# Optimization experiments

Hardware: AMD Instinct MI355X
Metric: run time of the kernel (lower is better)

## Reference

```python
import jax, jax.numpy as jnp
import numpy as np

T, TOPK = 512, 2
E, H, D = 8, 2816, 1024


def setup_inputs() -> dict:
    key = jax.random.key(0)
    k1, k2, k3, k4, k5 = jax.random.split(key, 5)
    x = jax.random.normal(k1, (T, D), dtype=jnp.float32)
    expert_indices = jax.random.randint(k2, (T, TOPK), 0, E, dtype=jnp.int64)
    w1 = jax.random.normal(k3, (E, H, D), dtype=jnp.float32)
    w2 = jax.random.normal(k4, (E, H, D), dtype=jnp.float32)
    w3 = jax.random.normal(k5, (E, H, D), dtype=jnp.float32)
    return {"x": x, "expert_indices": expert_indices, "w1": w1, "w2": w2, "w3": w3}


def reference(x, expert_indices, w1, w2, w3):
    # Math identical to: silu(x @ w1[e].T) * (x @ w3[e].T) @ w2[e] for e = expert_indices[t, a].
    # Computed densely over all experts (GEMM-friendly), then gathered per token,
    # which avoids materializing [T, a, H, D] gathered weight tensors.
    h1 = jax.nn.silu(jnp.einsum('ti,ehi->teh', x, w1))   # [T, E, H]
    h3 = jnp.einsum('ti,ehi->teh', x, w3)                # [T, E, H]
    out_all = jnp.einsum('teh,ehi->tei', h1 * h3, w2)    # [T, E, D]
    # gather the top_k selected experts per token -> [T, TOPK, D]
    idx = expert_indices[:, :, None]                     # [T, a, 1]
    expert_outs = jnp.take_along_axis(out_all, idx, axis=1)
    return expert_outs
```

## Files before the change

kernel.cpp:

```cpp
#include <hip/hip_runtime.h>


#define NEXP 8
#define HDIM 2816
#define DDIM 1024
#define NPAIR 1024

typedef unsigned int uint;
typedef unsigned short ushort;
typedef __attribute__((ext_vector_type(8))) short bf16x8;
typedef __attribute__((ext_vector_type(4))) float fvec4;
typedef __attribute__((ext_vector_type(4))) uint uvec4;

__device__ __forceinline__ ushort f2bf(float f) {
    uint u = __builtin_bit_cast(uint, f);
    u += 0x7fff + ((u >> 16) & 1);
    return (ushort)(u >> 16);
}
__device__ __forceinline__ uint pack2(float lo, float hi) {
    return (uint)f2bf(lo) | ((uint)f2bf(hi) << 16);
}
__device__ __forceinline__ uvec4 pack8(fvec4 a, fvec4 b) {
    uvec4 v;
    v.x = pack2(a.x, a.y); v.y = pack2(a.z, a.w);
    v.z = pack2(b.x, b.y); v.w = pack2(b.z, b.w);
    return v;
}

__device__ __forceinline__ void wg_sync_lds() {
    __builtin_amdgcn_sched_barrier(0);
    asm volatile("s_waitcnt lgkmcnt(0)" ::: "memory");
    __builtin_amdgcn_s_barrier();
    __builtin_amdgcn_sched_barrier(0);
}

__global__ __launch_bounds__(1024) void route_kernel(const int* __restrict__ idx,
                                                     int* __restrict__ counts,
                                                     int* __restrict__ lists) {
    int p = threadIdx.x;
    if (p < NEXP) counts[p] = 0;
    __syncthreads();
    int e = idx[p];
    int pos = atomicAdd(&counts[e], 1);
    lists[e * NPAIR + pos] = p;
}

#define LDB 68
#define NCH1 (DDIM / 64)

__global__ __launch_bounds__(512, 3) void h_mfma(const float* __restrict__ x,
                       const float* __restrict__ w1,
                       const float* __restrict__ w3,
                       const int* __restrict__ counts,
                       const int* __restrict__ lists,
                       ushort* __restrict__ hb) {
    const int e = blockIdx.x;
    const int cnt = counts[e];
    const int m0 = blockIdx.z * 128;
    if (m0 >= cnt) return;
    const int h0 = blockIdx.y * 64;

    __shared__ ushort sB1[2][64 * LDB];
    __shared__ ushort sB3[2][64 * LDB];
    __shared__ int sTok[128];
    __shared__ int sPairS[128];

    const int tid = threadIdx.x;
    if (tid < 128) {
        int m = m0 + tid;
        int mc = (m < cnt) ? m : (cnt - 1);
        int p = lists[e * NPAIR + mc];
        sTok[tid] = p >> 1;
        sPairS[tid] = (m < cnt) ? p : -1;
    }

    const int w = tid >> 6;
    const int lane = tid & 63;
    const int l16 = lane & 15;
    const int quad = lane >> 4;

    const int brow = tid >> 3;
    const int bc = (tid & 7) * 8;
    const float* pB1 = w1 + (size_t)e * HDIM * DDIM + (size_t)(h0 + brow) * DDIM + bc;
    const float* pB3 = w3 + (size_t)e * HDIM * DDIM + (size_t)(h0 + brow) * DDIM + bc;

    fvec4 pf[2][4];

#define P1_ISSUE(S, KC) do { \
    const float* q1 = pB1 + (KC) * 64; \
    const float* q3 = pB3 + (KC) * 64; \
    pf[S][0] = *(const fvec4*)q1;  pf[S][1] = *(const fvec4*)(q1 + 4); \
    pf[S][2] = *(const fvec4*)q3;  pf[S][3] = *(const fvec4*)(q3 + 4); \
} while (0)

#define P1_STAGE(S, B) do { \
    *(uvec4*)&sB1[B][brow * LDB + bc] = pack8(pf[S][0], pf[S][1]); \
    *(uvec4*)&sB3[B][brow * LDB + bc] = pack8(pf[S][2], pf[S][3]); \
} while (0)

    P1_ISSUE(0, 0);
    P1_ISSUE(1, 1);
    wg_sync_lds();
    const float* xA = x + (size_t)sTok[w * 16 + l16] * DDIM + quad * 8;

    fvec4 acc1[4], acc3[4];
    #pragma unroll
    for (int i = 0; i < 4; ++i) { acc1[i] = (fvec4)0.f; acc3[i] = (fvec4)0.f; }

    P1_STAGE(0, 0);
    wg_sync_lds();

#define P1_BODY(T, CUR) do { \
    const int kA = (T) * 64; \
    fvec4 a0 = *(const fvec4*)(xA + kA); \
    fvec4 a1 = *(const fvec4*)(xA + kA + 4); \
    fvec4 a2 = *(const fvec4*)(xA + kA + 32); \
    fvec4 a3 = *(const fvec4*)(xA + kA + 36); \
    if ((T) + 2 < NCH1) P1_ISSUE(CUR, (T) + 2); \
    bf16x8 af0 = __builtin_bit_cast(bf16x8, pack8(a0, a1)); \
    bf16x8 af1 = __builtin_bit_cast(bf16x8, pack8(a2, a3)); \
    _Pragma("unroll") \
    for (int ni = 0; ni < 4; ++ni) { \
        const int ro = (ni * 16 + l16) * LDB + quad * 8; \
        bf16x8 b10 = *(const bf16x8*)&sB1[CUR][ro]; \
        bf16x8 b30 = *(const bf16x8*)&sB3[CUR][ro]; \
        bf16x8 b11 = *(const bf16x8*)&sB1[CUR][ro + 32]; \
        bf16x8 b31 = *(const bf16x8*)&sB3[CUR][ro + 32]; \
        acc1[ni] = __builtin_amdgcn_mfma_f32_16x16x32_bf16(af0, b10, acc1[ni], 0, 0, 0); \
        acc3[ni] = __builtin_amdgcn_mfma_f32_16x16x32_bf16(af0, b30, acc3[ni], 0, 0, 0); \
        acc1[ni] = __builtin_amdgcn_mfma_f32_16x16x32_bf16(af1, b11, acc1[ni], 0, 0, 0); \
        acc3[ni] = __builtin_amdgcn_mfma_f32_16x16x32_bf16(af1, b31, acc3[ni], 0, 0, 0); \
    } \
    if ((T) + 1 < NCH1) { \
        P1_STAGE(CUR ^ 1, CUR ^ 1); \
        wg_sync_lds(); \
    } \
} while (0)

    for (int t = 0; t < NCH1; t += 2) {
        P1_BODY(t, 0);
        P1_BODY(t + 1, 1);
    }

    #pragma unroll
    for (int r = 0; r < 4; ++r) {
        int m = w * 16 + quad * 4 + r;
        int p = sPairS[m];
        if (p >= 0) {
            size_t base = (size_t)p * HDIM + h0;
            #pragma unroll
            for (int ni = 0; ni < 4; ++ni) {
                float a = acc1[ni][r];
                float g = acc3[ni][r];
                float s = a / (1.f + __expf(-a)) * g;
                hb[base + ni * 16 + l16] = f2bf(s);
            }
        }
    }
}

#define LDB2 68
#define NCH2 ((HDIM / 4) / 64)

__global__ __launch_bounds__(512, 3) void out_mfma(const float* __restrict__ w2,
                         const int* __restrict__ counts,
                         const int* __restrict__ lists,
                         const ushort* __restrict__ hb,
                         float* __restrict__ out) {
    const int e = blockIdx.x;
    const int cnt = counts[e];
    const int mb = blockIdx.z >> 2;
    const int sk = blockIdx.z & 3;
    const int m0 = mb * 128;
    if (m0 >= cnt) return;
    const int n0 = blockIdx.y * 64;
    const int kbase = sk * (HDIM / 4);

    __shared__ ushort sB[2][64 * LDB2];
    __shared__ int sPairC[128];
    __shared__ int sPairS[128];

    const int tid = threadIdx.x;
    if (tid < 128) {
        int m = m0 + tid;
        int mc = (m < cnt) ? m : (cnt - 1);
        int p = lists[e * NPAIR + mc];
        sPairC[tid] = p;
        sPairS[tid] = (m < cnt) ? p : -1;
    }

    const int w = tid >> 6;
    const int lane = tid & 63;
    const int l16 = lane & 15;
    const int quad = lane >> 4;
    const int kp = tid >> 4;
    const int n4 = tid & 15;

    const float* pW = w2 + (size_t)e * HDIM * DDIM
                         + (size_t)(kbase + 2 * kp) * DDIM + n0 + n4 * 4;

    fvec4 pw[2][2];

#define P2_ISSUE(S, KC) do { \
    const float* q = pW + (size_t)(KC) * 64 * DDIM; \
    pw[S][0] = *(const fvec4*)q; \
    pw[S][1] = *(const fvec4*)(q + DDIM); \
} while (0)

#define P2_STAGE(S, B) do { \
    _Pragma("unroll") \
    for (int j = 0; j < 4; ++j) \
        *(uint*)&sB[B][(n4 * 4 + j) * LDB2 + kp * 2] = pack2(pw[S][0][j], pw[S][1][j]); \
} while (0)

    P2_ISSUE(0, 0);
    P2_ISSUE(1, 1);
    wg_sync_lds();
    const ushort* pA = hb + (size_t)sPairC[w * 16 + l16] * HDIM + kbase + quad * 8;

    fvec4 acc[4];
    #pragma unroll
    for (int i = 0; i < 4; ++i) acc[i] = (fvec4)0.f;

    P2_STAGE(0, 0);
    wg_sync_lds();

#define P2_BODY(T, CUR) do { \
    const int kA = (T) * 64; \
    bf16x8 af0 = *(const bf16x8*)(pA + kA); \
    bf16x8 af1 = *(const bf16x8*)(pA + kA + 32); \
    if ((T) + 2 < NCH2) P2_ISSUE(CUR, (T) + 2); \
    _Pragma("unroll") \
    for (int ni = 0; ni < 4; ++ni) { \
        const int ro = (ni * 16 + l16) * LDB2 + quad * 8; \
        bf16x8 b0 = *(const bf16x8*)&sB[CUR][ro]; \
        bf16x8 b1 = *(const bf16x8*)&sB[CUR][ro + 32]; \
        acc[ni] = __builtin_amdgcn_mfma_f32_16x16x32_bf16(af0, b0, acc[ni], 0, 0, 0); \
        acc[ni] = __builtin_amdgcn_mfma_f32_16x16x32_bf16(af1, b1, acc[ni], 0, 0, 0); \
    } \
    if ((T) + 1 < NCH2) { \
        P2_STAGE(CUR ^ 1, CUR ^ 1); \
        wg_sync_lds(); \
    } \
} while (0)

    for (int t = 0; t < NCH2; t += 2) {
        P2_BODY(t, 0);
        if (t + 1 < NCH2) P2_BODY(t + 1, 1);
    }

    #pragma unroll
    for (int r = 0; r < 4; ++r) {
        int m = w * 16 + quad * 4 + r;
        int p = sPairS[m];
        if (p >= 0) {
            #pragma unroll
            for (int ni = 0; ni < 4; ++ni)
                atomicAdd(&out[(size_t)p * DDIM + n0 + ni * 16 + l16], acc[ni][r]);
        }
    }
}

extern "C" void kernel_launch(void* const* d_in, const int* in_sizes, int n_in,
                              void* d_out, int out_size, void* d_ws, size_t ws_size,
                              hipStream_t stream) {
    const float* x   = (const float*)d_in[0];
    const int*   idx = (const int*)d_in[1];
    const float* w1  = (const float*)d_in[2];
    const float* w2  = (const float*)d_in[3];
    const float* w3  = (const float*)d_in[4];
    float* out = (float*)d_out;

    char* ws = (char*)d_ws;
    int*    counts = (int*)ws;
    int*    lists  = (int*)(ws + 1024);
    ushort* hbuf   = (ushort*)(ws + 65536);

    hipMemsetAsync(out, 0, (size_t)out_size * sizeof(float), stream);
    route_kernel<<<1, NPAIR, 0, stream>>>(idx, counts, lists);
    h_mfma<<<dim3(NEXP, HDIM / 64, NPAIR / 128), 512, 0, stream>>>(
        x, w1, w3, counts, lists, hbuf);
    out_mfma<<<dim3(NEXP, DDIM / 64, (NPAIR / 128) * 4), 512, 0, stream>>>(
        w2, counts, lists, hbuf, out);
}
```

Before: 330.1 us.

## Stage A tiles through LDS and shrink N tiles to 32 in both MoE GEMMs

Both expert GEMM kernels now load the activation rows (x or the bf16 hidden buffer) cooperatively into a double-buffered LDS tile. Before, each wave read its A fragments straight from global memory. The output-column tile is halved from 64 to 32, which doubles the grid, and waves are rearranged as a 4x2 grid over M and N, each computing 32x16 per matrix. Launch bounds now ask for 4 blocks per CU instead of 3. The aim is more parallelism and coalesced A loads. The cost is that x/hb rows are reloaded twice as many times across blocks, and fewer MFMAs run per LDS read.

Result: slower. 345.2 us (+4.6%).

```diff
diff --git a/kernel.cpp b/kernel.cpp
--- a/kernel.cpp
+++ b/kernel.cpp
@@ -45,10 +45,11 @@
     lists[e * NPAIR + pos] = p;
 }
 
-#define LDB 68
+#define LDK 68
+
 #define NCH1 (DDIM / 64)
 
-__global__ __launch_bounds__(512, 3) void h_mfma(const float* __restrict__ x,
+__global__ __launch_bounds__(512, 4) void h_mfma(const float* __restrict__ x,
                        const float* __restrict__ w1,
                        const float* __restrict__ w3,
                        const int* __restrict__ counts,
@@ -58,10 +59,10 @@
     const int cnt = counts[e];
     const int m0 = blockIdx.z * 128;
     if (m0 >= cnt) return;
-    const int h0 = blockIdx.y * 64;
-
-    __shared__ ushort sB1[2][64 * LDB];
-    __shared__ ushort sB3[2][64 * LDB];
+    const int h0 = blockIdx.y * 32;
+
+    __shared__ ushort sA[2][128 * LDK];
+    __shared__ ushort sB[2][2][32 * LDK];
     __shared__ int sTok[128];
     __shared__ int sPairS[128];
 
@@ -73,64 +74,75 @@
         sTok[tid] = p >> 1;
         sPairS[tid] = (m < cnt) ? p : -1;
     }
+    wg_sync_lds();
+
+    const int arow = tid >> 2;
+    const int akg  = (tid & 3) * 16;
+    const float* aSrc = x + (size_t)sTok[arow] * DDIM + akg;
+
+    const int bmat = tid >> 8;
+    const int brow = (tid >> 3) & 31;
+    const int bkg  = (tid & 7) * 8;
+    const float* bSrc = (bmat ? w3 : w1) + (size_t)e * HDIM * DDIM
+                        + (size_t)(h0 + brow) * DDIM + bkg;
+
+    fvec4 pfA[2][4];
+    fvec4 pfB[2][2];
+
+#define P1_ISSUE(S, KC) do { \
+    const float* qa = aSrc + (KC) * 64; \
+    pfA[S][0] = *(const fvec4*)qa; \
+    pfA[S][1] = *(const fvec4*)(qa + 4); \
+    pfA[S][2] = *(const fvec4*)(qa + 8); \
+    pfA[S][3] = *(const fvec4*)(qa + 12); \
+    const float* qb = bSrc + (KC) * 64; \
+    pfB[S][0] = *(const fvec4*)qb; \
+    pfB[S][1] = *(const fvec4*)(qb + 4); \
+} while (0)
+
+#define P1_STAGE(S, B) do { \
+    *(uvec4*)&sA[B][arow * LDK + akg] = pack8(pfA[S][0], pfA[S][1]); \
+    *(uvec4*)&sA[B][arow * LDK + akg + 8] = pack8(pfA[S][2], pfA[S][3]); \
+    *(uvec4*)&sB[B][bmat][brow * LDK + bkg] = pack8(pfB[S][0], pfB[S][1]); \
+} while (0)
 
     const int w = tid >> 6;
+    const int wm = w & 3;
+    const int wh = w >> 2;
     const int lane = tid & 63;
     const int l16 = lane & 15;
     const int quad = lane >> 4;
 
-    const int brow = tid >> 3;
-    const int bc = (tid & 7) * 8;
-    const float* pB1 = w1 + (size_t)e * HDIM * DDIM + (size_t)(h0 + brow) * DDIM + bc;
-    const float* pB3 = w3 + (size_t)e * HDIM * DDIM + (size_t)(h0 + brow) * DDIM + bc;
-
-    fvec4 pf[2][4];
-
-#define P1_ISSUE(S, KC) do { \
-    const float* q1 = pB1 + (KC) * 64; \
-    const float* q3 = pB3 + (KC) * 64; \
-    pf[S][0] = *(const fvec4*)q1;  pf[S][1] = *(const fvec4*)(q1 + 4); \
-    pf[S][2] = *(const fvec4*)q3;  pf[S][3] = *(const fvec4*)(q3 + 4); \
-} while (0)
-
-#define P1_STAGE(S, B) do { \
-    *(uvec4*)&sB1[B][brow * LDB + bc] = pack8(pf[S][0], pf[S][1]); \
-    *(uvec4*)&sB3[B][brow * LDB + bc] = pack8(pf[S][2], pf[S][3]); \
-} while (0)
+    const int ar0 = (wm * 32 + l16) * LDK + quad * 8;
+    const int br0 = (wh * 16 + l16) * LDK + quad * 8;
+
+    fvec4 acc[2][2];
+    #pragma unroll
+    for (int i = 0; i < 2; ++i) { acc[i][0] = (fvec4)0.f; acc[i][1] = (fvec4)0.f; }
 
     P1_ISSUE(0, 0);
     P1_ISSUE(1, 1);
-    wg_sync_lds();
-    const float* xA = x + (size_t)sTok[w * 16 + l16] * DDIM + quad * 8;
-
-    fvec4 acc1[4], acc3[4];
-    #pragma unroll
-    for (int i = 0; i < 4; ++i) { acc1[i] = (fvec4)0.f; acc3[i] = (fvec4)0.f; }
-
     P1_STAGE(0, 0);
     wg_sync_lds();
 
 #define P1_BODY(T, CUR) do { \
-    const int kA = (T) * 64; \
-    fvec4 a0 = *(const fvec4*)(xA + kA); \
-    fvec4 a1 = *(const fvec4*)(xA + kA + 4); \
-    fvec4 a2 = *(const fvec4*)(xA + kA + 32); \
-    fvec4 a3 = *(const fvec4*)(xA + kA + 36); \
+    bf16x8 a00 = *(const bf16x8*)&sA[CUR][ar0]; \
+    bf16x8 a01 = *(const bf16x8*)&sA[CUR][ar0 + 32]; \
+    bf16x8 a10 = *(const bf16x8*)&sA[CUR][ar0 + 16 * LDK]; \
+    bf16x8 a11 = *(const bf16x8*)&sA[CUR][ar0 + 16 * LDK + 32]; \
+    bf16x8 b00 = *(const bf16x8*)&sB[CUR][0][br0]; \
+    bf16x8 b01 = *(const bf16x8*)&sB[CUR][0][br0 + 32]; \
+    bf16x8 b10 = *(const bf16x8*)&sB[CUR][1][br0]; \
+    bf16x8 b11 = *(const bf16x8*)&sB[CUR][1][br0 + 32]; \
     if ((T) + 2 < NCH1) P1_ISSUE(CUR, (T) + 2); \
-    bf16x8 af0 = __builtin_bit_cast(bf16x8, pack8(a0, a1)); \
-    bf16x8 af1 = __builtin_bit_cast(bf16x8, pack8(a2, a3)); \
-    _Pragma("unroll") \
-    for (int ni = 0; ni < 4; ++ni) { \
-        const int ro = (ni * 16 + l16) * LDB + quad * 8; \
-        bf16x8 b10 = *(const bf16x8*)&sB1[CUR][ro]; \
-        bf16x8 b30 = *(const bf16x8*)&sB3[CUR][ro]; \
-        bf16x8 b11 = *(const bf16x8*)&sB1[CUR][ro + 32]; \
-        bf16x8 b31 = *(const bf16x8*)&sB3[CUR][ro + 32]; \
-        acc1[ni] = __builtin_amdgcn_mfma_f32_16x16x32_bf16(af0, b10, acc1[ni], 0, 0, 0); \
-        acc3[ni] = __builtin_amdgcn_mfma_f32_16x16x32_bf16(af0, b30, acc3[ni], 0, 0, 0); \
-        acc1[ni] = __builtin_amdgcn_mfma_f32_16x16x32_bf16(af1, b11, acc1[ni], 0, 0, 0); \
-        acc3[ni] = __builtin_amdgcn_mfma_f32_16x16x32_bf16(af1, b31, acc3[ni], 0, 0, 0); \
-    } \
+    acc[0][0] = __builtin_amdgcn_mfma_f32_16x16x32_bf16(a00, b00, acc[0][0], 0, 0, 0); \
+    acc[0][1] = __builtin_amdgcn_mfma_f32_16x16x32_bf16(a00, b10, acc[0][1], 0, 0, 0); \
+    acc[1][0] = __builtin_amdgcn_mfma_f32_16x16x32_bf16(a10, b00, acc[1][0], 0, 0, 0); \
+    acc[1][1] = __builtin_amdgcn_mfma_f32_16x16x32_bf16(a10, b10, acc[1][1], 0, 0, 0); \
+    acc[0][0] = __builtin_amdgcn_mfma_f32_16x16x32_bf16(a01, b01, acc[0][0], 0, 0, 0); \
+    acc[0][1] = __builtin_amdgcn_mfma_f32_16x16x32_bf16(a01, b11, acc[0][1], 0, 0, 0); \
+    acc[1][0] = __builtin_amdgcn_mfma_f32_16x16x32_bf16(a11, b01, acc[1][0], 0, 0, 0); \
+    acc[1][1] = __builtin_amdgcn_mfma_f32_16x16x32_bf16(a11, b11, acc[1][1], 0, 0, 0); \
     if ((T) + 1 < NCH1) { \
         P1_STAGE(CUR ^ 1, CUR ^ 1); \
         wg_sync_lds(); \
@@ -143,26 +155,24 @@
     }
 
     #pragma unroll
-    for (int r = 0; r < 4; ++r) {
-        int m = w * 16 + quad * 4 + r;
-        int p = sPairS[m];
-        if (p >= 0) {
-            size_t base = (size_t)p * HDIM + h0;
-            #pragma unroll
-            for (int ni = 0; ni < 4; ++ni) {
-                float a = acc1[ni][r];
-                float g = acc3[ni][r];
+    for (int mi = 0; mi < 2; ++mi) {
+        #pragma unroll
+        for (int r = 0; r < 4; ++r) {
+            int mrow = wm * 32 + mi * 16 + quad * 4 + r;
+            int p = sPairS[mrow];
+            if (p >= 0) {
+                float a = acc[mi][0][r];
+                float g = acc[mi][1][r];
                 float s = a / (1.f + __expf(-a)) * g;
-                hb[base + ni * 16 + l16] = f2bf(s);
+                hb[(size_t)p * HDIM + h0 + wh * 16 + l16] = f2bf(s);
             }
         }
     }
 }
 
-#define LDB2 68
 #define NCH2 ((HDIM / 4) / 64)
 
-__global__ __launch_bounds__(512, 3) void out_mfma(const float* __restrict__ w2,
+__global__ __launch_bounds__(512, 4) void out_mfma(const float* __restrict__ w2,
                          const int* __restrict__ counts,
                          const int* __restrict__ lists,
                          const ushort* __restrict__ hb,
@@ -173,10 +183,11 @@
     const int sk = blockIdx.z & 3;
     const int m0 = mb * 128;
     if (m0 >= cnt) return;
-    const int n0 = blockIdx.y * 64;
+    const int n0 = blockIdx.y * 32;
     const int kbase = sk * (HDIM / 4);
 
-    __shared__ ushort sB[2][64 * LDB2];
+    __shared__ ushort sA[2][128 * LDK];
+    __shared__ ushort sB[2][32 * LDK];
     __shared__ int sPairC[128];
     __shared__ int sPairS[128];
 
@@ -188,56 +199,71 @@
         sPairC[tid] = p;
         sPairS[tid] = (m < cnt) ? p : -1;
     }
+    wg_sync_lds();
+
+    const int arow = tid >> 2;
+    const int akg  = (tid & 3) * 16;
+    const ushort* aSrc = hb + (size_t)sPairC[arow] * HDIM + kbase + akg;
+
+    const int bkp = (tid >> 3) & 31;
+    const int bdg = tid & 7;
+    const float* bSrc = w2 + (size_t)e * HDIM * DDIM
+                        + (size_t)(kbase + 2 * bkp) * DDIM + n0 + bdg * 4;
+
+    uvec4 pfA[2][2];
+    fvec4 pfB[2][2];
+
+#define P2_ISSUE(S, KC) do { \
+    const ushort* qa = aSrc + (KC) * 64; \
+    pfA[S][0] = *(const uvec4*)qa; \
+    pfA[S][1] = *(const uvec4*)(qa + 8); \
+    if (tid < 256) { \
+        const float* qb = bSrc + (size_t)(KC) * 64 * DDIM; \
+        pfB[S][0] = *(const fvec4*)qb; \
+        pfB[S][1] = *(const fvec4*)(qb + DDIM); \
+    } \
+} while (0)
+
+#define P2_STAGE(S, B) do { \
+    *(uvec4*)&sA[B][arow * LDK + akg] = pfA[S][0]; \
+    *(uvec4*)&sA[B][arow * LDK + akg + 8] = pfA[S][1]; \
+    if (tid < 256) { \
+        _Pragma("unroll") \
+        for (int j = 0; j < 4; ++j) \
+            *(uint*)&sB[B][(bdg * 4 + j) * LDK + bkp * 2] = pack2(pfB[S][0][j], pfB[S][1][j]); \
+    } \
+} while (0)
 
     const int w = tid >> 6;
+    const int wm = w & 3;
+    const int wh = w >> 2;
     const int lane = tid & 63;
     const int l16 = lane & 15;
     const int quad = lane >> 4;
-    const int kp = tid >> 4;
-    const int n4 = tid & 15;
-
-    const float* pW = w2 + (size_t)e * HDIM * DDIM
-                         + (size_t)(kbase + 2 * kp) * DDIM + n0 + n4 * 4;
-
-    fvec4 pw[2][2];
-
-#define P2_ISSUE(S, KC) do { \
-    const float* q = pW + (size_t)(KC) * 64 * DDIM; \
-    pw[S][0] = *(const fvec4*)q; \
-    pw[S][1] = *(const fvec4*)(q + DDIM); \
-} while (0)
-
-#define P2_STAGE(S, B) do { \
-    _Pragma("unroll") \
-    for (int j = 0; j < 4; ++j) \
-        *(uint*)&sB[B][(n4 * 4 + j) * LDB2 + kp * 2] = pack2(pw[S][0][j], pw[S][1][j]); \
-} while (0)
+
+    const int ar0 = (wm * 32 + l16) * LDK + quad * 8;
+    const int br0 = (wh * 16 + l16) * LDK + quad * 8;
+
+    fvec4 acc[2];
+    acc[0] = (fvec4)0.f; acc[1] = (fvec4)0.f;
 
     P2_ISSUE(0, 0);
     P2_ISSUE(1, 1);
-    wg_sync_lds();
-    const ushort* pA = hb + (size_t)sPairC[w * 16 + l16] * HDIM + kbase + quad * 8;
-
-    fvec4 acc[4];
-    #pragma unroll
-    for (int i = 0; i < 4; ++i) acc[i] = (fvec4)0.f;
-
     P2_STAGE(0, 0);
     wg_sync_lds();
 
 #define P2_BODY(T, CUR) do { \
-    const int kA = (T) * 64; \
-    bf16x8 af0 = *(const bf16x8*)(pA + kA); \
-    bf16x8 af1 = *(const bf16x8*)(pA + kA + 32); \
+    bf16x8 a00 = *(const bf16x8*)&sA[CUR][ar0]; \
+    bf16x8 a01 = *(const bf16x8*)&sA[CUR][ar0 + 32]; \
+    bf16x8 a10 = *(const bf16x8*)&sA[CUR][ar0 + 16 * LDK]; \
+    bf16x8 a11 = *(const bf16x8*)&sA[CUR][ar0 + 16 * LDK + 32]; \
+    bf16x8 b0 = *(const bf16x8*)&sB[CUR][br0]; \
+    bf16x8 b1 = *(const bf16x8*)&sB[CUR][br0 + 32]; \
     if ((T) + 2 < NCH2) P2_ISSUE(CUR, (T) + 2); \
-    _Pragma("unroll") \
-    for (int ni = 0; ni < 4; ++ni) { \
-        const int ro = (ni * 16 + l16) * LDB2 + quad * 8; \
-        bf16x8 b0 = *(const bf16x8*)&sB[CUR][ro]; \
-        bf16x8 b1 = *(const bf16x8*)&sB[CUR][ro + 32]; \
-        acc[ni] = __builtin_amdgcn_mfma_f32_16x16x32_bf16(af0, b0, acc[ni], 0, 0, 0); \
-        acc[ni] = __builtin_amdgcn_mfma_f32_16x16x32_bf16(af1, b1, acc[ni], 0, 0, 0); \
-    } \
+    acc[0] = __builtin_amdgcn_mfma_f32_16x16x32_bf16(a00, b0, acc[0], 0, 0, 0); \
+    acc[1] = __builtin_amdgcn_mfma_f32_16x16x32_bf16(a10, b0, acc[1], 0, 0, 0); \
+    acc[0] = __builtin_amdgcn_mfma_f32_16x16x32_bf16(a01, b1, acc[0], 0, 0, 0); \
+    acc[1] = __builtin_amdgcn_mfma_f32_16x16x32_bf16(a11, b1, acc[1], 0, 0, 0); \
     if ((T) + 1 < NCH2) { \
         P2_STAGE(CUR ^ 1, CUR ^ 1); \
         wg_sync_lds(); \
@@ -250,13 +276,13 @@
     }
 
     #pragma unroll
-    for (int r = 0; r < 4; ++r) {
-        int m = w * 16 + quad * 4 + r;
-        int p = sPairS[m];
-        if (p >= 0) {
-            #pragma unroll
-            for (int ni = 0; ni < 4; ++ni)
-                atomicAdd(&out[(size_t)p * DDIM + n0 + ni * 16 + l16], acc[ni][r]);
+    for (int mi = 0; mi < 2; ++mi) {
+        #pragma unroll
+        for (int r = 0; r < 4; ++r) {
+            int mrow = wm * 32 + mi * 16 + quad * 4 + r;
+            int p = sPairS[mrow];
+            if (p >= 0)
+                atomicAdd(&out[(size_t)p * DDIM + n0 + wh * 16 + l16], acc[mi][r]);
         }
     }
 }
@@ -278,8 +304,8 @@
 
     hipMemsetAsync(out, 0, (size_t)out_size * sizeof(float), stream);
     route_kernel<<<1, NPAIR, 0, stream>>>(idx, counts, lists);
-    h_mfma<<<dim3(NEXP, HDIM / 64, NPAIR / 128), 512, 0, stream>>>(
+    h_mfma<<<dim3(NEXP, HDIM / 32, NPAIR / 128), 512, 0, stream>>>(
         x, w1, w3, counts, lists, hbuf);
-    out_mfma<<<dim3(NEXP, DDIM / 64, (NPAIR / 128) * 4), 512, 0, stream>>>(
+    out_mfma<<<dim3(NEXP, DDIM / 32, (NPAIR / 128) * 4), 512, 0, stream>>>(
         w2, counts, lists, hbuf, out);
 }
```
